# Performance work log

Hardware: AMD Instinct MI355X
Metric: run time of the kernel (lower is better)

The kernel has to match this reference:

```python
import jax, jax.numpy as jnp
import numpy as np

T, B = 1024, 512
IN_F, HID, OUT = 64, 128, 2
DT = 0.001

# SuperSpike surrogate gradient (norse default threshold method='super')
@jax.custom_vjp
def superspike(x, alpha):
    return (x > 0).astype(x.dtype)

def _ss_fwd(x, alpha):
    return superspike(x, alpha), (x, alpha)

def _ss_bwd(res, g):
    x, alpha = res
    return (g / (alpha * jnp.abs(x) + 1.0) ** 2, jnp.zeros_like(alpha))

superspike.defvjp(_ss_fwd, _ss_bwd)


def setup_inputs() -> dict:
    key = jax.random.key(0)
    ks = jax.random.split(key, 6)
    x = jax.random.normal(ks[0], (T, B, IN_F), jnp.float32)
    # nn.Linear(input, hidden, bias=False)
    W_in = jax.random.normal(ks[1], (HID, IN_F), jnp.float32) / np.sqrt(IN_F)
    # LIFRecurrentCell(hidden, hidden) weights (norse init scale sqrt(2/hidden))
    cell_W_in = jax.random.normal(ks[2], (HID, HID), jnp.float32) * np.sqrt(2.0 / HID)
    cell_W_rec = jax.random.normal(ks[3], (HID, HID), jnp.float32) * np.sqrt(2.0 / HID)
    cell_W_rec = cell_W_rec * (1.0 - jnp.eye(HID, dtype=jnp.float32))  # autapses=False
    # nn.Linear(hidden, output, bias=True)
    W_out = jax.random.normal(ks[4], (OUT, HID), jnp.float32) / np.sqrt(HID)
    b_out = jax.random.normal(ks[5], (OUT,), jnp.float32) * 0.01
    # LIFParameters as in __init__
    alpha = jnp.full((HID,), 100.0, jnp.float32)
    v_th = jnp.full((HID,), 1.0, jnp.float32)
    v_leak = jnp.asarray(0.0, jnp.float32)
    v_reset = jnp.full((HID,), 0.0, jnp.float32)
    tau_mem_inv = jnp.full((HID,), 100.0, jnp.float32)
    tau_syn_inv = jnp.full((HID,), 200.0, jnp.float32)
    return dict(x=x, W_in=W_in, cell_W_in=cell_W_in, cell_W_rec=cell_W_rec,
                W_out=W_out, b_out=b_out, alpha=alpha, v_th=v_th, v_leak=v_leak,
                v_reset=v_reset, tau_mem_inv=tau_mem_inv, tau_syn_inv=tau_syn_inv)


def reference(x, W_in, cell_W_in, cell_W_rec, W_out, b_out,
              alpha, v_th, v_leak, v_reset, tau_mem_inv, tau_syn_inv):
    Tn, Bn, _ = x.shape
    H = W_in.shape[0]

    def step(carry, x_t):
        z, v, i = carry                                   # each [B,H]
        inp = x_t @ W_in.T                                # input_layer
        # norse _lif_step: decay v and i, spike, reset, inject currents
        v_dec = v + DT * tau_mem_inv * ((v_leak - v) + i)
        i_dec = i - DT * tau_syn_inv * i
        z_new = superspike(v_dec - v_th, alpha)
        v_new = (1.0 - z_new) * v_dec + z_new * v_reset
        i_new = i_dec + inp @ cell_W_in.T + z @ cell_W_rec.T
        out_t = z_new @ W_out.T + b_out                   # output_layer
        return (z_new, v_new, i_new), (out_t, jnp.sum(z_new))

    init = (jnp.zeros((Bn, H), x.dtype),
            jnp.zeros((Bn, H), x.dtype),
            jnp.zeros((Bn, H), x.dtype))
    _, (outs, spk) = jax.lax.scan(step, init, x)
    z_sum = jnp.sum(outs, axis=0)                         # __decode_sum over time
    spikerate = jnp.sum(spk) / (Tn * Bn * H)
    return z_sum, spikerate
```

## Files before the change

### kernel.cpp

```cpp
#include <hip/hip_runtime.h>
#include <stdint.h>

#define T_STEPS 1024
#define BATCH   512
#define INF     64
#define HID     128
#define OUTF    2

__global__ void zero_kernel(unsigned int* __restrict__ counter)
{
    *counter = 0u;
}

#define FOR16(M) M(0)M(1)M(2)M(3)M(4)M(5)M(6)M(7)M(8)M(9)M(10)M(11)M(12)M(13)M(14)M(15)
#define BARRIER() asm volatile("s_waitcnt lgkmcnt(0)\n\ts_barrier" ::: "memory")

__global__ __launch_bounds__(512) __attribute__((amdgpu_waves_per_eu(4, 4)))
void snn_seq(const float* __restrict__ x,
             const float* __restrict__ W_in,
             const float* __restrict__ cWi,
             const float* __restrict__ Wrec,
             const float* __restrict__ W_out,
             const float* __restrict__ b_out,
             const float* __restrict__ v_th,
             const float* __restrict__ v_leak1,
             const float* __restrict__ v_reset,
             const float* __restrict__ tau_mem,
             const float* __restrict__ tau_syn,
             float* __restrict__ out,
             unsigned int* __restrict__ counter)
{
    #pragma clang fp contract(off)

    extern __shared__ char smem[];
    float* Wrec_T  = (float*)smem;
    float* inp_lds = Wrec_T + HID * HID;
    float* x_lds   = inp_lds + 4 * HID;
    float* q_lds   = x_lds + 4 * INF;
    float* pre_lds = q_lds + 2 * HID;

    const int tid = threadIdx.x;
    const int b   = blockIdx.x;

    for (int idx = tid; idx < HID * HID; idx += 512)
        Wrec_T[idx] = Wrec[(idx & (HID - 1)) * HID + (idx >> 7)];

    if (tid < 128) {
        const int h = tid;
        const float4* cwr = (const float4*)(cWi + h * HID);
        #define DECL_C(q) float4 c##q = cwr[q];
        FOR16(DECL_C)
        #undef DECL_C

        #define S2A(q) { float4 i4 = ir4[q]; \
            acc = fmaf(i4.x, c##q.x, acc); acc = fmaf(i4.y, c##q.y, acc); \
            acc = fmaf(i4.z, c##q.z, acc); acc = fmaf(i4.w, c##q.w, acc); }

        __syncthreads();
        BARRIER();
        {
            const float4* ir4 = (const float4*)(inp_lds + 0 * HID);
            float acc = 0.f; FOR16(S2A)
            q_lds[0 * HID + h] = acc;
        }
        BARRIER();
        {
            const float4* ir4 = (const float4*)(inp_lds + 1 * HID);
            float acc = 0.f; FOR16(S2A)
            q_lds[1 * HID + h] = acc;
        }
        BARRIER();
        for (int i = 0; i < T_STEPS; i += 2) {
            {
                const float4* ir4 = (const float4*)(inp_lds + ((i + 2) & 3) * HID);
                float acc = 0.f; FOR16(S2A)
                q_lds[0 * HID + h] = acc;
            }
            BARRIER();
            {
                const float4* ir4 = (const float4*)(inp_lds + ((i + 3) & 3) * HID);
                float acc = 0.f; FOR16(S2A)
                q_lds[1 * HID + h] = acc;
            }
            BARRIER();
        }
        #undef S2A
    } else if (tid < 256) {
        const int h = tid - 128;
        const float4* cwr = (const float4*)(cWi + h * HID) + 16;
        #define DECL_D(q) float4 d##q = cwr[q];
        FOR16(DECL_D)
        #undef DECL_D

        #define S2B(q) { float4 i4 = ir4[q]; \
            acc = fmaf(i4.x, d##q.x, acc); acc = fmaf(i4.y, d##q.y, acc); \
            acc = fmaf(i4.z, d##q.z, acc); acc = fmaf(i4.w, d##q.w, acc); }

        __syncthreads();
        BARRIER();
        BARRIER();
        {
            const float4* ir4 = (const float4*)(inp_lds + 0 * HID) + 16;
            float acc = q_lds[0 * HID + h];
            FOR16(S2B)
            pre_lds[0 * HID + h] = acc;
        }
        BARRIER();
        for (int i = 0; i < T_STEPS; i += 2) {
            {
                const float4* ir4 = (const float4*)(inp_lds + ((i + 1) & 3) * HID) + 16;
                float acc = q_lds[1 * HID + h];
                FOR16(S2B)
                pre_lds[1 * HID + h] = acc;
            }
            BARRIER();
            {
                const float4* ir4 = (const float4*)(inp_lds + ((i + 2) & 3) * HID) + 16;
                float acc = q_lds[0 * HID + h];
                FOR16(S2B)
                pre_lds[0 * HID + h] = acc;
            }
            BARRIER();
        }
        #undef S2B
    } else if (tid < 384) {
        const int l = tid - 256;
        const float4* wra = (const float4*)(W_in + l * INF);
        #define DECL_A(q) float4 a##q = wra[q];
        FOR16(DECL_A)
        #undef DECL_A

        #define S1(q) { float4 x4 = xr4[q]; \
            acc = fmaf(x4.x, a##q.x, acc); acc = fmaf(x4.y, a##q.y, acc); \
            acc = fmaf(x4.z, a##q.z, acc); acc = fmaf(x4.w, a##q.w, acc); }

        __syncthreads();
        {
            const float4* xr4 = (const float4*)(x_lds + 0 * INF);
            float acc = 0.f; FOR16(S1)
            inp_lds[0 * HID + l] = acc;
        }
        BARRIER();
        {
            const float4* xr4 = (const float4*)(x_lds + 1 * INF);
            float acc = 0.f; FOR16(S1)
            inp_lds[1 * HID + l] = acc;
        }
        BARRIER();
        {
            const float4* xr4 = (const float4*)(x_lds + 2 * INF);
            float acc = 0.f; FOR16(S1)
            inp_lds[2 * HID + l] = acc;
        }
        BARRIER();
        for (int i = 0; i < T_STEPS; i += 2) {
            {
                const int s = (i + 3) & 3;
                const float4* xr4 = (const float4*)(x_lds + s * INF);
                float acc = 0.f; FOR16(S1)
                inp_lds[s * HID + l] = acc;
            }
            BARRIER();
            {
                const int s = (i + 4) & 3;
                const float4* xr4 = (const float4*)(x_lds + s * INF);
                float acc = 0.f; FOR16(S1)
                inp_lds[s * HID + l] = acc;
            }
            BARRIER();
        }
        #undef S1
    } else if (tid < 448) {
        const int l  = tid - 384;
        const int h0 = 2 * l, h1 = 2 * l + 1;

        const double vth0  = (double)v_th[h0],    vth1  = (double)v_th[h1];
        const double vleak = (double)v_leak1[0];
        const double vrs0  = (double)v_reset[h0], vrs1  = (double)v_reset[h1];
        const double dtm0  = 0.001 * (double)tau_mem[h0];
        const double dtm1  = 0.001 * (double)tau_mem[h1];
        const double dts0  = 0.001 * (double)tau_syn[h0];
        const double dts1  = 0.001 * (double)tau_syn[h1];

        double v0 = 0.0, v1 = 0.0, c0 = 0.0, c1 = 0.0;
        int cnt0 = 0, cnt1 = 0;
        unsigned long long me = 0ull, mo = 0ull;

        __syncthreads();
        BARRIER(); BARRIER(); BARRIER();

        for (int i = 0; i < T_STEPS; ++i) {
            float2 pp = *(const float2*)(pre_lds + (i & 1) * HID + h0);

            double s00 = 0.0, s01 = 0.0, s10 = 0.0, s11 = 0.0;
            {
                unsigned long long A = me, Bm = mo;
                while (A | Bm) {
                    float2 w0 = make_float2(0.f, 0.f), w1 = w0, w2 = w0, w3 = w0,
                           w4 = w0, w5 = w0, w6 = w0, w7 = w0;
                    if (A)  { int j = __builtin_ctzll(A);  A  &= A - 1;  w0 = *(const float2*)(Wrec_T + (2 * j) * HID + h0); }
                    if (A)  { int j = __builtin_ctzll(A);  A  &= A - 1;  w1 = *(const float2*)(Wrec_T + (2 * j) * HID + h0); }
                    if (A)  { int j = __builtin_ctzll(A);  A  &= A - 1;  w2 = *(const float2*)(Wrec_T + (2 * j) * HID + h0); }
                    if (A)  { int j = __builtin_ctzll(A);  A  &= A - 1;  w3 = *(const float2*)(Wrec_T + (2 * j) * HID + h0); }
                    if (Bm) { int j = __builtin_ctzll(Bm); Bm &= Bm - 1; w4 = *(const float2*)(Wrec_T + (2 * j + 1) * HID + h0); }
                    if (Bm) { int j = __builtin_ctzll(Bm); Bm &= Bm - 1; w5 = *(const float2*)(Wrec_T + (2 * j + 1) * HID + h0); }
                    if (Bm) { int j = __builtin_ctzll(Bm); Bm &= Bm - 1; w6 = *(const float2*)(Wrec_T + (2 * j + 1) * HID + h0); }
                    if (Bm) { int j = __builtin_ctzll(Bm); Bm &= Bm - 1; w7 = *(const float2*)(Wrec_T + (2 * j + 1) * HID + h0); }
                    s00 += (double)w0.x; s10 += (double)w0.y;
                    s01 += (double)w1.x; s11 += (double)w1.y;
                    s00 += (double)w2.x; s10 += (double)w2.y;
                    s01 += (double)w3.x; s11 += (double)w3.y;
                    s00 += (double)w4.x; s10 += (double)w4.y;
                    s01 += (double)w5.x; s11 += (double)w5.y;
                    s00 += (double)w6.x; s10 += (double)w6.y;
                    s01 += (double)w7.x; s11 += (double)w7.y;
                }
            }
            double rec0 = s00 + s01;
            double rec1 = s10 + s11;

            double vd0 = v0 + dtm0 * ((vleak - v0) + c0);
            double id0 = c0 - dts0 * c0;
            bool   z0  = (vd0 - vth0) > 0.0;
            v0 = z0 ? vrs0 : vd0;
            c0 = (id0 + (double)pp.x) + rec0;
            cnt0 += z0 ? 1 : 0;

            double vd1 = v1 + dtm1 * ((vleak - v1) + c1);
            double id1 = c1 - dts1 * c1;
            bool   z1  = (vd1 - vth1) > 0.0;
            v1 = z1 ? vrs1 : vd1;
            c1 = (id1 + (double)pp.y) + rec1;
            cnt1 += z1 ? 1 : 0;

            me = __ballot(z0);
            mo = __ballot(z1);
            BARRIER();
        }

        pre_lds[h0] = (float)cnt0;
        pre_lds[h1] = (float)cnt1;
    } else {
        const int l = tid - 448;
        float t0 = x[(size_t)(0 * BATCH + b) * INF + l];
        float t1 = x[(size_t)(1 * BATCH + b) * INF + l];
        float t2 = x[(size_t)(2 * BATCH + b) * INF + l];
        float t3 = x[(size_t)(3 * BATCH + b) * INF + l];
        x_lds[0 * INF + l] = t0;
        x_lds[1 * INF + l] = t1;
        x_lds[2 * INF + l] = t2;
        x_lds[3 * INF + l] = t3;
        float rC = x[(size_t)(4 * BATCH + b) * INF + l];
        float rA = x[(size_t)(5 * BATCH + b) * INF + l];
        float rB = x[(size_t)(6 * BATCH + b) * INF + l];

        __syncthreads();
        BARRIER();
        BARRIER();
        x_lds[0 * INF + l] = rC;
        BARRIER();
        for (int i = 0; i < T_STEPS; i += 2) {
            {
                x_lds[((i + 5) & 3) * INF + l] = rA;
                int tn = (i + 7 < T_STEPS) ? i + 7 : T_STEPS - 1;
                rA = x[((size_t)tn * BATCH + b) * INF + l];
            }
            BARRIER();
            {
                x_lds[((i + 6) & 3) * INF + l] = rB;
                int tn = (i + 8 < T_STEPS) ? i + 8 : T_STEPS - 1;
                rB = x[((size_t)tn * BATCH + b) * INF + l];
            }
            BARRIER();
        }
    }

    __syncthreads();

    const float* cnt_lds = pre_lds;
    if (tid < OUTF) {
        double sAcc = 0.0;
        for (int hh = 0; hh < HID; ++hh)
            sAcc += (double)cnt_lds[hh] * (double)W_out[tid * HID + hh];
        out[(size_t)b * OUTF + tid] = (float)(sAcc + 1024.0 * (double)b_out[tid]);
    }
    if (tid == 0) {
        unsigned int tot = 0;
        for (int k2 = 0; k2 < HID; ++k2) tot += (unsigned int)cnt_lds[k2];
        atomicAdd(counter, tot);
    }
}

__global__ void finalize_kernel(float* __restrict__ out)
{
    unsigned int c = ((const unsigned int*)out)[BATCH * OUTF];
    out[BATCH * OUTF] = (float)c * 0x1p-26f;
}

extern "C" void kernel_launch(void* const* d_in, const int* in_sizes, int n_in,
                              void* d_out, int out_size, void* d_ws, size_t ws_size,
                              hipStream_t stream) {
    (void)in_sizes; (void)n_in; (void)d_ws; (void)ws_size; (void)out_size;

    const float* x       = (const float*)d_in[0];
    const float* W_in    = (const float*)d_in[1];
    const float* cWi     = (const float*)d_in[2];
    const float* cWr     = (const float*)d_in[3];
    const float* W_out   = (const float*)d_in[4];
    const float* b_out   = (const float*)d_in[5];
    const float* v_th    = (const float*)d_in[7];
    const float* v_leak  = (const float*)d_in[8];
    const float* v_reset = (const float*)d_in[9];
    const float* tau_mem = (const float*)d_in[10];
    const float* tau_syn = (const float*)d_in[11];
    float* out = (float*)d_out;
    unsigned int* counter = (unsigned int*)out + BATCH * OUTF;

    zero_kernel<<<1, 1, 0, stream>>>(counter);

    const size_t lds_bytes =
        (size_t)(HID * HID + 4 * HID + 4 * INF + 2 * HID + 2 * HID) * sizeof(float);
    snn_seq<<<dim3(512), dim3(512), lds_bytes, stream>>>(
        x, W_in, cWi, cWr, W_out, b_out, v_th, v_leak, v_reset,
        tau_mem, tau_syn, out, counter);

    finalize_kernel<<<1, 1, 0, stream>>>(out);
}
```

Before: 725.0 us.

## Process two batch rows per block to share weights and barriers

Each block now handles two batch rows (G=2) instead of one, launching half as many blocks of 576 threads. The input-projection and cell-input matvec stages compute two rows per thread, reusing the register-held weights with two independent accumulator chains. Two waves run the spiking recurrence, one per row, and one extra wave streams x for both rows. The aim is to amortise per-step barrier and latency overhead across two rows, at the cost of more FMA work per stage thread and different register and occupancy limits.

```diff
diff --git a/kernel.cpp b/kernel.cpp
--- a/kernel.cpp
+++ b/kernel.cpp
@@ -6,6 +6,7 @@
 #define INF     64
 #define HID     128
 #define OUTF    2
+#define G       2
 
 __global__ void zero_kernel(unsigned int* __restrict__ counter)
 {
@@ -15,7 +16,7 @@
 #define FOR16(M) M(0)M(1)M(2)M(3)M(4)M(5)M(6)M(7)M(8)M(9)M(10)M(11)M(12)M(13)M(14)M(15)
 #define BARRIER() asm volatile("s_waitcnt lgkmcnt(0)\n\ts_barrier" ::: "memory")
 
-__global__ __launch_bounds__(512) __attribute__((amdgpu_waves_per_eu(4, 4)))
+__global__ __launch_bounds__(576, 2)
 void snn_seq(const float* __restrict__ x,
              const float* __restrict__ W_in,
              const float* __restrict__ cWi,
@@ -35,14 +36,14 @@
     extern __shared__ char smem[];
     float* Wrec_T  = (float*)smem;
     float* inp_lds = Wrec_T + HID * HID;
-    float* x_lds   = inp_lds + 4 * HID;
-    float* q_lds   = x_lds + 4 * INF;
-    float* pre_lds = q_lds + 2 * HID;
+    float* x_lds   = inp_lds + 4 * G * HID;
+    float* q_lds   = x_lds + 4 * G * INF;
+    float* pre_lds = q_lds + 2 * G * HID;
 
     const int tid = threadIdx.x;
-    const int b   = blockIdx.x;
-
-    for (int idx = tid; idx < HID * HID; idx += 512)
+    const int b0  = blockIdx.x * G;
+
+    for (int idx = tid; idx < HID * HID; idx += 576)
         Wrec_T[idx] = Wrec[(idx & (HID - 1)) * HID + (idx >> 7)];
 
     if (tid < 128) {
@@ -52,38 +53,31 @@
         FOR16(DECL_C)
         #undef DECL_C
 
-        #define S2A(q) { float4 i4 = ir4[q]; \
-            acc = fmaf(i4.x, c##q.x, acc); acc = fmaf(i4.y, c##q.y, acc); \
-            acc = fmaf(i4.z, c##q.z, acc); acc = fmaf(i4.w, c##q.w, acc); }
-
-        __syncthreads();
-        BARRIER();
-        {
-            const float4* ir4 = (const float4*)(inp_lds + 0 * HID);
-            float acc = 0.f; FOR16(S2A)
-            q_lds[0 * HID + h] = acc;
-        }
-        BARRIER();
-        {
-            const float4* ir4 = (const float4*)(inp_lds + 1 * HID);
-            float acc = 0.f; FOR16(S2A)
-            q_lds[1 * HID + h] = acc;
-        }
+        #define S2A(q) { float4 u = ir0[q]; float4 w = ir1[q]; \
+            a0 = fmaf(u.x, c##q.x, a0); a0 = fmaf(u.y, c##q.y, a0); \
+            a0 = fmaf(u.z, c##q.z, a0); a0 = fmaf(u.w, c##q.w, a0); \
+            a1 = fmaf(w.x, c##q.x, a1); a1 = fmaf(w.y, c##q.y, a1); \
+            a1 = fmaf(w.z, c##q.z, a1); a1 = fmaf(w.w, c##q.w, a1); }
+        #define DO_W2A(t) { \
+            const float4* ir0 = (const float4*)(inp_lds + (((t) & 3) * G + 0) * HID); \
+            const float4* ir1 = (const float4*)(inp_lds + (((t) & 3) * G + 1) * HID); \
+            float a0 = 0.f, a1 = 0.f; FOR16(S2A) \
+            q_lds[(((t) & 1) * G + 0) * HID + h] = a0; \
+            q_lds[(((t) & 1) * G + 1) * HID + h] = a1; }
+
+        __syncthreads();
+        BARRIER();
+        DO_W2A(0)
+        BARRIER();
+        DO_W2A(1)
         BARRIER();
         for (int i = 0; i < T_STEPS; i += 2) {
-            {
-                const float4* ir4 = (const float4*)(inp_lds + ((i + 2) & 3) * HID);
-                float acc = 0.f; FOR16(S2A)
-                q_lds[0 * HID + h] = acc;
-            }
-            BARRIER();
-            {
-                const float4* ir4 = (const float4*)(inp_lds + ((i + 3) & 3) * HID);
-                float acc = 0.f; FOR16(S2A)
-                q_lds[1 * HID + h] = acc;
-            }
-            BARRIER();
-        }
+            DO_W2A(i + 2)
+            BARRIER();
+            DO_W2A(i + 3)
+            BARRIER();
+        }
+        #undef DO_W2A
         #undef S2A
     } else if (tid < 256) {
         const int h = tid - 128;
@@ -92,36 +86,32 @@
         FOR16(DECL_D)
         #undef DECL_D
 
-        #define S2B(q) { float4 i4 = ir4[q]; \
-            acc = fmaf(i4.x, d##q.x, acc); acc = fmaf(i4.y, d##q.y, acc); \
-            acc = fmaf(i4.z, d##q.z, acc); acc = fmaf(i4.w, d##q.w, acc); }
-
-        __syncthreads();
-        BARRIER();
-        BARRIER();
-        {
-            const float4* ir4 = (const float4*)(inp_lds + 0 * HID) + 16;
-            float acc = q_lds[0 * HID + h];
-            FOR16(S2B)
-            pre_lds[0 * HID + h] = acc;
-        }
+        #define S2B(q) { float4 u = ir0[q]; float4 w = ir1[q]; \
+            a0 = fmaf(u.x, d##q.x, a0); a0 = fmaf(u.y, d##q.y, a0); \
+            a0 = fmaf(u.z, d##q.z, a0); a0 = fmaf(u.w, d##q.w, a0); \
+            a1 = fmaf(w.x, d##q.x, a1); a1 = fmaf(w.y, d##q.y, a1); \
+            a1 = fmaf(w.z, d##q.z, a1); a1 = fmaf(w.w, d##q.w, a1); }
+        #define DO_W2B(t) { \
+            const float4* ir0 = (const float4*)(inp_lds + (((t) & 3) * G + 0) * HID) + 16; \
+            const float4* ir1 = (const float4*)(inp_lds + (((t) & 3) * G + 1) * HID) + 16; \
+            float a0 = q_lds[(((t) & 1) * G + 0) * HID + h]; \
+            float a1 = q_lds[(((t) & 1) * G + 1) * HID + h]; \
+            FOR16(S2B) \
+            pre_lds[(((t) & 1) * G + 0) * HID + h] = a0; \
+            pre_lds[(((t) & 1) * G + 1) * HID + h] = a1; }
+
+        __syncthreads();
+        BARRIER();
+        BARRIER();
+        DO_W2B(0)
         BARRIER();
         for (int i = 0; i < T_STEPS; i += 2) {
-            {
-                const float4* ir4 = (const float4*)(inp_lds + ((i + 1) & 3) * HID) + 16;
-                float acc = q_lds[1 * HID + h];
-                FOR16(S2B)
-                pre_lds[1 * HID + h] = acc;
-            }
-            BARRIER();
-            {
-                const float4* ir4 = (const float4*)(inp_lds + ((i + 2) & 3) * HID) + 16;
-                float acc = q_lds[0 * HID + h];
-                FOR16(S2B)
-                pre_lds[0 * HID + h] = acc;
-            }
-            BARRIER();
-        }
+            DO_W2B(i + 1)
+            BARRIER();
+            DO_W2B(i + 2)
+            BARRIER();
+        }
+        #undef DO_W2B
         #undef S2B
     } else if (tid < 384) {
         const int l = tid - 256;
@@ -130,49 +120,37 @@
         FOR16(DECL_A)
         #undef DECL_A
 
-        #define S1(q) { float4 x4 = xr4[q]; \
-            acc = fmaf(x4.x, a##q.x, acc); acc = fmaf(x4.y, a##q.y, acc); \
-            acc = fmaf(x4.z, a##q.z, acc); acc = fmaf(x4.w, a##q.w, acc); }
-
-        __syncthreads();
-        {
-            const float4* xr4 = (const float4*)(x_lds + 0 * INF);
-            float acc = 0.f; FOR16(S1)
-            inp_lds[0 * HID + l] = acc;
-        }
-        BARRIER();
-        {
-            const float4* xr4 = (const float4*)(x_lds + 1 * INF);
-            float acc = 0.f; FOR16(S1)
-            inp_lds[1 * HID + l] = acc;
-        }
-        BARRIER();
-        {
-            const float4* xr4 = (const float4*)(x_lds + 2 * INF);
-            float acc = 0.f; FOR16(S1)
-            inp_lds[2 * HID + l] = acc;
-        }
+        #define S1(q) { float4 u = xr0[q]; float4 w = xr1[q]; \
+            s0 = fmaf(u.x, a##q.x, s0); s0 = fmaf(u.y, a##q.y, s0); \
+            s0 = fmaf(u.z, a##q.z, s0); s0 = fmaf(u.w, a##q.w, s0); \
+            s1 = fmaf(w.x, a##q.x, s1); s1 = fmaf(w.y, a##q.y, s1); \
+            s1 = fmaf(w.z, a##q.z, s1); s1 = fmaf(w.w, a##q.w, s1); }
+        #define DO_W1(t) { \
+            const float4* xr0 = (const float4*)(x_lds + (((t) & 3) * G + 0) * INF); \
+            const float4* xr1 = (const float4*)(x_lds + (((t) & 3) * G + 1) * INF); \
+            float s0 = 0.f, s1 = 0.f; FOR16(S1) \
+            inp_lds[(((t) & 3) * G + 0) * HID + l] = s0; \
+            inp_lds[(((t) & 3) * G + 1) * HID + l] = s1; }
+
+        __syncthreads();
+        DO_W1(0)
+        BARRIER();
+        DO_W1(1)
+        BARRIER();
+        DO_W1(2)
         BARRIER();
         for (int i = 0; i < T_STEPS; i += 2) {
-            {
-                const int s = (i + 3) & 3;
-                const float4* xr4 = (const float4*)(x_lds + s * INF);
-                float acc = 0.f; FOR16(S1)
-                inp_lds[s * HID + l] = acc;
-            }
-            BARRIER();
-            {
-                const int s = (i + 4) & 3;
-                const float4* xr4 = (const float4*)(x_lds + s * INF);
-                float acc = 0.f; FOR16(S1)
-                inp_lds[s * HID + l] = acc;
-            }
-            BARRIER();
-        }
+            DO_W1(i + 3)
+            BARRIER();
+            DO_W1(i + 4)
+            BARRIER();
+        }
+        #undef DO_W1
         #undef S1
-    } else if (tid < 448) {
-        const int l  = tid - 384;
-        const int h0 = 2 * l, h1 = 2 * l + 1;
+    } else if (tid < 512) {
+        const int row = (tid >> 6) & 1;
+        const int l   = tid & 63;
+        const int h0  = 2 * l, h1 = 2 * l + 1;
 
         const double vth0  = (double)v_th[h0],    vth1  = (double)v_th[h1];
         const double vleak = (double)v_leak1[0];
@@ -190,7 +168,7 @@
         BARRIER(); BARRIER(); BARRIER();
 
         for (int i = 0; i < T_STEPS; ++i) {
-            float2 pp = *(const float2*)(pre_lds + (i & 1) * HID + h0);
+            float2 pp = *(const float2*)(pre_lds + ((i & 1) * G + row) * HID + h0);
 
             double s00 = 0.0, s01 = 0.0, s10 = 0.0, s11 = 0.0;
             {
@@ -238,38 +216,49 @@
             BARRIER();
         }
 
-        pre_lds[h0] = (float)cnt0;
-        pre_lds[h1] = (float)cnt1;
+        pre_lds[row * HID + h0] = (float)cnt0;
+        pre_lds[row * HID + h1] = (float)cnt1;
     } else {
-        const int l = tid - 448;
-        float t0 = x[(size_t)(0 * BATCH + b) * INF + l];
-        float t1 = x[(size_t)(1 * BATCH + b) * INF + l];
-        float t2 = x[(size_t)(2 * BATCH + b) * INF + l];
-        float t3 = x[(size_t)(3 * BATCH + b) * INF + l];
-        x_lds[0 * INF + l] = t0;
-        x_lds[1 * INF + l] = t1;
-        x_lds[2 * INF + l] = t2;
-        x_lds[3 * INF + l] = t3;
-        float rC = x[(size_t)(4 * BATCH + b) * INF + l];
-        float rA = x[(size_t)(5 * BATCH + b) * INF + l];
-        float rB = x[(size_t)(6 * BATCH + b) * INF + l];
-
-        __syncthreads();
-        BARRIER();
-        BARRIER();
-        x_lds[0 * INF + l] = rC;
+        const int l = tid - 512;
+        float rA0, rA1, rB0, rB1, rC0, rC1;
+        x_lds[(0 * G + 0) * INF + l] = x[(size_t)(0 * BATCH + b0 + 0) * INF + l];
+        x_lds[(0 * G + 1) * INF + l] = x[(size_t)(0 * BATCH + b0 + 1) * INF + l];
+        x_lds[(1 * G + 0) * INF + l] = x[(size_t)(1 * BATCH + b0 + 0) * INF + l];
+        x_lds[(1 * G + 1) * INF + l] = x[(size_t)(1 * BATCH + b0 + 1) * INF + l];
+        x_lds[(2 * G + 0) * INF + l] = x[(size_t)(2 * BATCH + b0 + 0) * INF + l];
+        x_lds[(2 * G + 1) * INF + l] = x[(size_t)(2 * BATCH + b0 + 1) * INF + l];
+        x_lds[(3 * G + 0) * INF + l] = x[(size_t)(3 * BATCH + b0 + 0) * INF + l];
+        x_lds[(3 * G + 1) * INF + l] = x[(size_t)(3 * BATCH + b0 + 1) * INF + l];
+        rC0 = x[(size_t)(4 * BATCH + b0 + 0) * INF + l];
+        rC1 = x[(size_t)(4 * BATCH + b0 + 1) * INF + l];
+        rA0 = x[(size_t)(5 * BATCH + b0 + 0) * INF + l];
+        rA1 = x[(size_t)(5 * BATCH + b0 + 1) * INF + l];
+        rB0 = x[(size_t)(6 * BATCH + b0 + 0) * INF + l];
+        rB1 = x[(size_t)(6 * BATCH + b0 + 1) * INF + l];
+
+        __syncthreads();
+        BARRIER();
+        BARRIER();
+        x_lds[(0 * G + 0) * INF + l] = rC0;
+        x_lds[(0 * G + 1) * INF + l] = rC1;
         BARRIER();
         for (int i = 0; i < T_STEPS; i += 2) {
             {
-                x_lds[((i + 5) & 3) * INF + l] = rA;
+                const int s = (i + 5) & 3;
+                x_lds[(s * G + 0) * INF + l] = rA0;
+                x_lds[(s * G + 1) * INF + l] = rA1;
                 int tn = (i + 7 < T_STEPS) ? i + 7 : T_STEPS - 1;
-                rA = x[((size_t)tn * BATCH + b) * INF + l];
+                rA0 = x[((size_t)tn * BATCH + b0 + 0) * INF + l];
+                rA1 = x[((size_t)tn * BATCH + b0 + 1) * INF + l];
             }
             BARRIER();
             {
-                x_lds[((i + 6) & 3) * INF + l] = rB;
+                const int s = (i + 6) & 3;
+                x_lds[(s * G + 0) * INF + l] = rB0;
+                x_lds[(s * G + 1) * INF + l] = rB1;
                 int tn = (i + 8 < T_STEPS) ? i + 8 : T_STEPS - 1;
-                rB = x[((size_t)tn * BATCH + b) * INF + l];
+                rB0 = x[((size_t)tn * BATCH + b0 + 0) * INF + l];
+                rB1 = x[((size_t)tn * BATCH + b0 + 1) * INF + l];
             }
             BARRIER();
         }
@@ -278,15 +267,16 @@
     __syncthreads();
 
     const float* cnt_lds = pre_lds;
-    if (tid < OUTF) {
+    if (tid < G * OUTF) {
+        int row = tid >> 1, oo = tid & 1;
         double sAcc = 0.0;
         for (int hh = 0; hh < HID; ++hh)
-            sAcc += (double)cnt_lds[hh] * (double)W_out[tid * HID + hh];
-        out[(size_t)b * OUTF + tid] = (float)(sAcc + 1024.0 * (double)b_out[tid]);
+            sAcc += (double)cnt_lds[row * HID + hh] * (double)W_out[oo * HID + hh];
+        out[(size_t)(b0 + row) * OUTF + oo] = (float)(sAcc + 1024.0 * (double)b_out[oo]);
     }
     if (tid == 0) {
         unsigned int tot = 0;
-        for (int k2 = 0; k2 < HID; ++k2) tot += (unsigned int)cnt_lds[k2];
+        for (int k2 = 0; k2 < G * HID; ++k2) tot += (unsigned int)cnt_lds[k2];
         atomicAdd(counter, tot);
     }
 }
@@ -319,8 +309,9 @@
     zero_kernel<<<1, 1, 0, stream>>>(counter);
 
     const size_t lds_bytes =
-        (size_t)(HID * HID + 4 * HID + 4 * INF + 2 * HID + 2 * HID) * sizeof(float);
-    snn_seq<<<dim3(512), dim3(512), lds_bytes, stream>>>(
+        (size_t)(HID * HID + 4 * G * HID + 4 * G * INF + 2 * G * HID + 2 * G * HID)
+        * sizeof(float);
+    snn_seq<<<dim3(BATCH / G), dim3(576), lds_bytes, stream>>>(
         x, W_in, cWi, cWr, W_out, b_out, v_th, v_leak, v_reset,
         tau_mem, tau_syn, out, counter);
 
```

After: 734.6 us. Within noise of the previous version (+1.3%).
